# Performance work log

Hardware: AMD Instinct MI355X
Metric: run time of the kernel (lower is better)

## Reference

```python
import jax, jax.numpy as jnp
import numpy as np

# spconv.SparseConv4d(C_in, 16, (1,3,3,3), stride=1, padding=0) on spatial_shape [1000,1000,40]:
# leading kernel dim is size 1, so this is a regular (non-submanifold) 3D sparse conv,
# valid padding -> output spatial shape (998, 998, 38). Implemented as gather-GEMM-scatter:
# input point p contributes feat(p) @ W[k] to output coord p - offset[k] for each of 27 taps.

N = 200000
C_IN = 64
C_OUT = 16
K = 3
OUT_SP = (998, 998, 38)  # 1000-3+1, 1000-3+1, 40-3+1
SENT = OUT_SP[0] * OUT_SP[1] * OUT_SP[2]  # sentinel linear index for invalid taps


def setup_inputs() -> dict:
    key = jax.random.key(0)
    k1, k2, k3, k4, k5, k6 = jax.random.split(key, 6)
    feats = jax.random.normal(k1, (N, C_IN), dtype=jnp.float32)
    x = jax.random.randint(k2, (N,), 0, 1000, dtype=jnp.int32)
    y = jax.random.randint(k3, (N,), 0, 1000, dtype=jnp.int32)
    z = jax.random.randint(k4, (N,), 0, 40, dtype=jnp.int32)
    coords = jnp.stack([jnp.zeros((N,), jnp.int32), x, y, z], axis=1)  # [N,4] (b,x,y,z)
    fan_in = C_IN * K * K * K
    W = jax.random.normal(k5, (K * K * K, C_IN, C_OUT), dtype=jnp.float32) / np.sqrt(fan_in)
    bias = jax.random.normal(k6, (C_OUT,), dtype=jnp.float32) * 0.01
    return {"input": feats, "coords": coords, "W": W, "bias": bias}


def reference(input, coords, W, bias):
    # kernel tap offsets, C-order over (kx,ky,kz) in [0,3)^3 -> [27,3]
    off = jnp.stack(
        jnp.meshgrid(jnp.arange(K), jnp.arange(K), jnp.arange(K), indexing="ij"),
        axis=-1,
    ).reshape(K * K * K, 3).astype(jnp.int32)
    xyz = coords[:, 1:4]                              # [N,3]
    oc = xyz[:, None, :] - off[None, :, :]            # [N,27,3] output coord per tap
    out_sp = jnp.array(OUT_SP, dtype=jnp.int32)
    valid = jnp.all((oc >= 0) & (oc < out_sp), axis=-1)  # [N,27]
    lin = oc[..., 0] * (OUT_SP[1] * OUT_SP[2]) + oc[..., 1] * OUT_SP[2] + oc[..., 2]
    lin = jnp.where(valid, lin, SENT).reshape(-1)     # [N*27]

    # gather-GEMM: per-tap GEMM over all active voxels
    contrib = jnp.einsum("nc,kco->nko", input, W)     # [N,27,16]
    contrib = jnp.where(valid[..., None], contrib, 0.0).reshape(-1, C_OUT)

    NK = N * (K * K * K)
    uniq, inv = jnp.unique(lin, return_inverse=True, size=NK, fill_value=SENT)
    inv = inv.reshape(-1)
    # scatter-add into unique output sites
    out = jax.ops.segment_sum(contrib, inv, num_segments=NK)  # [NK,16]
    cnt = jax.ops.segment_sum(valid.reshape(-1).astype(jnp.int32), inv, num_segments=NK)
    out = out + jnp.where(cnt[:, None] > 0, bias[None, :], 0.0)
    return out, uniq
```

## Files before the change

### kernel.cpp

```cpp
#include <hip/hip_runtime.h>

#define N_PTS   200000
#define CIN     64
#define COUT    16
#define KK      27
#define SXD     998
#define SYD     998
#define SZD     38
#define STRX    (SYD*SZD)
#define SENTV   (SXD*SYD*SZD)
#define NKTOT   (N_PTS*KK)
#define NWORDS  ((SENTV+31)/32)
#define NCHUNK  ((NWORDS+255)/256)

__global__ void mark_kernel(const int* __restrict__ coords, unsigned* __restrict__ bitmap,
                            unsigned* __restrict__ multi) {
    int n = blockIdx.x * blockDim.x + threadIdx.x;
    if (n >= N_PTS) return;
    int x = coords[n*4+1], y = coords[n*4+2], z = coords[n*4+3];
    #pragma unroll
    for (int m = 0; m < KK; m++) {
        int ox = x - (m/9), oy = y - ((m/3)%3), oz = z - (m%3);
        if (ox >= 0 && ox < SXD && oy >= 0 && oy < SYD && oz >= 0 && oz < SZD) {
            int lin = ox*STRX + oy*SZD + oz;
            unsigned b = 1u << (lin & 31);
            unsigned old = atomicOr(&bitmap[lin >> 5], b);
            if (old & b) atomicOr(&multi[lin >> 5], b);
        }
    }
}

__global__ void chunk_sums_kernel(const unsigned* __restrict__ bitmap, unsigned* __restrict__ csums) {
    int w = blockIdx.x * 256 + threadIdx.x;
    unsigned c = (w < NWORDS) ? (unsigned)__popc(bitmap[w]) : 0u;
    __shared__ unsigned s[256];
    s[threadIdx.x] = c;
    __syncthreads();
    for (int off = 128; off > 0; off >>= 1) {
        if (threadIdx.x < off) s[threadIdx.x] += s[threadIdx.x + off];
        __syncthreads();
    }
    if (threadIdx.x == 0) csums[blockIdx.x] = s[0];
}

__global__ void scan_chunks_kernel(const unsigned* __restrict__ csums,
                                   unsigned* __restrict__ cprefix,
                                   unsigned* __restrict__ Uptr) {
    __shared__ unsigned s[256];
    __shared__ unsigned run_s;
    if (threadIdx.x == 0) run_s = 0;
    __syncthreads();
    for (int base = 0; base < NCHUNK; base += 256) {
        int i = base + threadIdx.x;
        unsigned v = (i < NCHUNK) ? csums[i] : 0u;
        s[threadIdx.x] = v;
        __syncthreads();
        for (int off = 1; off < 256; off <<= 1) {
            unsigned t = (threadIdx.x >= off) ? s[threadIdx.x - off] : 0u;
            __syncthreads();
            s[threadIdx.x] += t;
            __syncthreads();
        }
        unsigned run = run_s;
        if (i < NCHUNK) cprefix[i] = run + s[threadIdx.x] - v;
        unsigned tile_total = s[255];
        __syncthreads();
        if (threadIdx.x == 255) run_s = run + tile_total;
        __syncthreads();
    }
    if (threadIdx.x == 0) Uptr[0] = run_s;
}

__global__ void word_prefix_kernel(const unsigned* __restrict__ bitmap,
                                   const unsigned* __restrict__ cprefix,
                                   unsigned* __restrict__ wprefix) {
    int w = blockIdx.x * 256 + threadIdx.x;
    unsigned v = (w < NWORDS) ? (unsigned)__popc(bitmap[w]) : 0u;
    __shared__ unsigned s[256];
    s[threadIdx.x] = v;
    __syncthreads();
    for (int off = 1; off < 256; off <<= 1) {
        unsigned t = (threadIdx.x >= off) ? s[threadIdx.x - off] : 0u;
        __syncthreads();
        s[threadIdx.x] += t;
        __syncthreads();
    }
    if (w < NWORDS) wprefix[w] = cprefix[blockIdx.x] + s[threadIdx.x] - v;
}

__global__ void fill_out_kernel(float* __restrict__ out, const float* __restrict__ bias,
                                const unsigned* __restrict__ Uptr) {
    unsigned U = Uptr[0];
    unsigned i = blockIdx.x * blockDim.x + threadIdx.x;
    if (i >= (unsigned)NKTOT * 4u) return;
    unsigned row = i >> 2;
    int q = i & 3;
    float4 v;
    if (row < U) v = ((const float4*)bias)[q];
    else         v = make_float4(0.f, 0.f, 0.f, 0.f);
    ((float4*)out)[i] = v;
}

__global__ void fill_uniq_kernel(float* __restrict__ uniq) {
    unsigned i = blockIdx.x * blockDim.x + threadIdx.x;
    if (i < (unsigned)NKTOT) uniq[i] = (float)SENTV;
}

__global__ void write_uniq_kernel(const unsigned* __restrict__ bitmap,
                                  const unsigned* __restrict__ wprefix,
                                  float* __restrict__ uniq) {
    int w = blockIdx.x * 256 + threadIdx.x;
    if (w >= NWORDS) return;
    unsigned bits = bitmap[w];
    unsigned r = wprefix[w];
    while (bits) {
        int b = __ffs(bits) - 1;
        bits &= bits - 1;
        uniq[r++] = (float)(w * 32 + b);
    }
}

__launch_bounds__(256)
__global__ void scatter_mm_kernel(const float* __restrict__ feats,
                                  const int* __restrict__ coords,
                                  const float* __restrict__ W,
                                  const float* __restrict__ bias,
                                  const unsigned* __restrict__ bitmap,
                                  const unsigned* __restrict__ multi,
                                  const unsigned* __restrict__ wprefix,
                                  float* __restrict__ out) {
    int n = blockIdx.x * 256 + threadIdx.x;
    if (n >= N_PTS) return;
    int x = coords[n*4+1], y = coords[n*4+2], z = coords[n*4+3];

    float4 f[CIN/4];
    const float4* fin4 = (const float4*)(feats + (size_t)n * CIN);
    #pragma unroll
    for (int i = 0; i < CIN/4; i++) f[i] = fin4[i];

    #pragma unroll 1
    for (int m = 0; m < KK; m++) {
        int ox = x - (m/9), oy = y - ((m/3)%3), oz = z - (m%3);
        if (ox < 0 || ox >= SXD || oy < 0 || oy >= SYD || oz < 0 || oz >= SZD) continue;
        int lin = ox*STRX + oy*SZD + oz;
        unsigned word = (unsigned)lin >> 5, bit = (unsigned)lin & 31u;
        unsigned rank = wprefix[word] + (unsigned)__popc(bitmap[word] & ((1u << bit) - 1u));
        bool is_multi = (multi[word] >> bit) & 1u;

        const float* wk = W + (size_t)m * CIN * COUT;
        float acc[COUT];
        #pragma unroll
        for (int o = 0; o < COUT; o++) acc[o] = 0.f;
        #pragma unroll
        for (int c4 = 0; c4 < CIN/4; c4++) {
            float4 fv = f[c4];
            const float* wrow = wk + c4 * 4 * COUT;
            #pragma unroll
            for (int o = 0; o < COUT; o++) {
                acc[o] += fv.x * wrow[o] + fv.y * wrow[COUT + o]
                        + fv.z * wrow[2*COUT + o] + fv.w * wrow[3*COUT + o];
            }
        }

        float* dst = out + (size_t)rank * COUT;
        if (!is_multi) {
            #pragma unroll
            for (int q = 0; q < 4; q++) {
                float4 v;
                v.x = acc[q*4+0] + bias[q*4+0];
                v.y = acc[q*4+1] + bias[q*4+1];
                v.z = acc[q*4+2] + bias[q*4+2];
                v.w = acc[q*4+3] + bias[q*4+3];
                ((float4*)dst)[q] = v;
            }
        } else {
            #pragma unroll
            for (int o = 0; o < COUT; o++) atomicAdd(dst + o, acc[o]);
        }
    }
}

extern "C" void kernel_launch(void* const* d_in, const int* in_sizes, int n_in,
                              void* d_out, int out_size, void* d_ws, size_t ws_size,
                              hipStream_t stream) {
    const float* feats  = (const float*)d_in[0];
    const int*   coords = (const int*)d_in[1];
    const float* W      = (const float*)d_in[2];
    const float* bias   = (const float*)d_in[3];
    float* out  = (float*)d_out;
    float* uniq = out + (size_t)NKTOT * COUT;

    unsigned* ws      = (unsigned*)d_ws;
    unsigned* bitmap  = ws;
    unsigned* multi   = ws + NWORDS;
    unsigned* wprefix = ws + 2 * (size_t)NWORDS;
    unsigned* csums   = ws + 3 * (size_t)NWORDS;
    unsigned* cprefix = csums + NCHUNK;
    unsigned* Uptr    = cprefix + NCHUNK;

    size_t needed = ((size_t)3 * NWORDS + 2 * NCHUNK + 1) * sizeof(unsigned);
    bool have_multi = ws_size >= needed;
    if (!have_multi) {
        multi   = bitmap;
        wprefix = ws + NWORDS;
        csums   = ws + 2 * (size_t)NWORDS;
        cprefix = csums + NCHUNK;
        Uptr    = cprefix + NCHUNK;
        hipMemsetAsync(bitmap, 0, (size_t)NWORDS * sizeof(unsigned), stream);
    } else {
        hipMemsetAsync(bitmap, 0, 2 * (size_t)NWORDS * sizeof(unsigned), stream);
    }

    mark_kernel<<<(N_PTS + 255) / 256, 256, 0, stream>>>(coords, bitmap, multi);
    chunk_sums_kernel<<<NCHUNK, 256, 0, stream>>>(bitmap, csums);
    scan_chunks_kernel<<<1, 256, 0, stream>>>(csums, cprefix, Uptr);
    word_prefix_kernel<<<NCHUNK, 256, 0, stream>>>(bitmap, cprefix, wprefix);
    fill_out_kernel<<<(NKTOT * 4 + 255) / 256, 256, 0, stream>>>(out, bias, Uptr);
    fill_uniq_kernel<<<(NKTOT + 255) / 256, 256, 0, stream>>>(uniq);
    write_uniq_kernel<<<NCHUNK, 256, 0, stream>>>(bitmap, wprefix, uniq);
    scatter_mm_kernel<<<(N_PTS + 255) / 256, 256, 0, stream>>>(
        feats, coords, W, bias, bitmap, multi, wprefix, out);
}
```

Baseline: 1.410 ms.

## Batch z-taps into word masks, write only tail and multi-site bias, shrink scatter blocks

The mark kernel now sets all z-taps of an (x,y) column with one or two atomicOr calls on a contiguous bit mask, instead of one atomic per tap. The full-output bias fill is replaced by two writes: bias goes only to rows hit more than once, which are seeded inside write_uniq, and a tail kernel zero-fills rows past U with nontemporal stores. Single-hit rows are written directly by the scatter kernel. That kernel now uses 64-thread blocks, vector coordinate loads, nontemporal feature loads and stores, and bias held in registers. The aim is to cut atomic traffic and avoid rewriting the roughly 345 MB output twice, at the cost of relying on every single-hit row being written later by the scatter kernel.

Result: faster. 1.253 ms (-11.1%).

```diff
diff --git a/kernel.cpp b/kernel.cpp
--- a/kernel.cpp
+++ b/kernel.cpp
@@ -13,19 +13,39 @@
 #define NWORDS  ((SENTV+31)/32)
 #define NCHUNK  ((NWORDS+255)/256)
 
+typedef float f32x4 __attribute__((ext_vector_type(4)));
+
 __global__ void mark_kernel(const int* __restrict__ coords, unsigned* __restrict__ bitmap,
                             unsigned* __restrict__ multi) {
     int n = blockIdx.x * blockDim.x + threadIdx.x;
     if (n >= N_PTS) return;
-    int x = coords[n*4+1], y = coords[n*4+2], z = coords[n*4+3];
-    #pragma unroll
-    for (int m = 0; m < KK; m++) {
-        int ox = x - (m/9), oy = y - ((m/3)%3), oz = z - (m%3);
-        if (ox >= 0 && ox < SXD && oy >= 0 && oy < SYD && oz >= 0 && oz < SZD) {
-            int lin = ox*STRX + oy*SZD + oz;
-            unsigned b = 1u << (lin & 31);
-            unsigned old = atomicOr(&bitmap[lin >> 5], b);
-            if (old & b) atomicOr(&multi[lin >> 5], b);
+    int4 c = ((const int4*)coords)[n];
+    int x = c.y, y = c.z, z = c.w;
+    int zlo = z - 2; if (zlo < 0) zlo = 0;
+    int zhi = z;     if (zhi > SZD - 1) zhi = SZD - 1;
+    unsigned nb = (unsigned)(zhi - zlo + 1);
+    unsigned mseed = (1u << nb) - 1u;
+    #pragma unroll
+    for (int dx = 0; dx < 3; dx++) {
+        int ox = x - dx;
+        if (ox < 0 || ox >= SXD) continue;
+        #pragma unroll
+        for (int dy = 0; dy < 3; dy++) {
+            int oy = y - dy;
+            if (oy < 0 || oy >= SYD) continue;
+            int lin = ox*STRX + oy*SZD + zlo;
+            unsigned w = (unsigned)lin >> 5;
+            unsigned b = (unsigned)lin & 31u;
+            unsigned lowm = mseed << b;
+            unsigned old = atomicOr(&bitmap[w], lowm);
+            unsigned col = old & lowm;
+            if (col) atomicOr(&multi[w], col);
+            if (b + nb > 32u) {
+                unsigned highm = mseed >> (32u - b);
+                unsigned old2 = atomicOr(&bitmap[w+1], highm);
+                unsigned col2 = old2 & highm;
+                if (col2) atomicOr(&multi[w+1], col2);
+            }
         }
     }
 }
@@ -106,21 +126,48 @@
     if (i < (unsigned)NKTOT) uniq[i] = (float)SENTV;
 }
 
+__global__ void tail_kernel(float* __restrict__ out, float* __restrict__ uniq,
+                            const unsigned* __restrict__ Uptr) {
+    unsigned U = Uptr[0];
+    unsigned i = blockIdx.x * blockDim.x + threadIdx.x;
+    if (i >= (unsigned)NKTOT || i < U) return;
+    f32x4 z4 = {0.f, 0.f, 0.f, 0.f};
+    f32x4* dst = (f32x4*)(out + (size_t)i * COUT);
+    #pragma unroll
+    for (int q = 0; q < 4; q++) __builtin_nontemporal_store(z4, dst + q);
+    __builtin_nontemporal_store((float)SENTV, uniq + i);
+}
+
 __global__ void write_uniq_kernel(const unsigned* __restrict__ bitmap,
+                                  const unsigned* __restrict__ multi,
                                   const unsigned* __restrict__ wprefix,
-                                  float* __restrict__ uniq) {
+                                  float* __restrict__ uniq,
+                                  float* __restrict__ out,
+                                  const float* __restrict__ bias,
+                                  int do_bias) {
     int w = blockIdx.x * 256 + threadIdx.x;
     if (w >= NWORDS) return;
     unsigned bits = bitmap[w];
+    if (!bits) return;
+    unsigned mbits = do_bias ? multi[w] : 0u;
+    f32x4 bv[4];
+    #pragma unroll
+    for (int q = 0; q < 4; q++) bv[q] = ((const f32x4*)bias)[q];
     unsigned r = wprefix[w];
     while (bits) {
         int b = __ffs(bits) - 1;
         bits &= bits - 1;
-        uniq[r++] = (float)(w * 32 + b);
-    }
-}
-
-__launch_bounds__(256)
+        uniq[r] = (float)(w * 32 + b);
+        if ((mbits >> b) & 1u) {
+            f32x4* dst = (f32x4*)(out + (size_t)r * COUT);
+            #pragma unroll
+            for (int q = 0; q < 4; q++) __builtin_nontemporal_store(bv[q], dst + q);
+        }
+        r++;
+    }
+}
+
+__launch_bounds__(64)
 __global__ void scatter_mm_kernel(const float* __restrict__ feats,
                                   const int* __restrict__ coords,
                                   const float* __restrict__ W,
@@ -129,14 +176,19 @@
                                   const unsigned* __restrict__ multi,
                                   const unsigned* __restrict__ wprefix,
                                   float* __restrict__ out) {
-    int n = blockIdx.x * 256 + threadIdx.x;
+    int n = blockIdx.x * 64 + threadIdx.x;
     if (n >= N_PTS) return;
-    int x = coords[n*4+1], y = coords[n*4+2], z = coords[n*4+3];
-
-    float4 f[CIN/4];
-    const float4* fin4 = (const float4*)(feats + (size_t)n * CIN);
-    #pragma unroll
-    for (int i = 0; i < CIN/4; i++) f[i] = fin4[i];
+    int4 cc = ((const int4*)coords)[n];
+    int x = cc.y, y = cc.z, z = cc.w;
+
+    f32x4 f[CIN/4];
+    const f32x4* fin4 = (const f32x4*)(feats + (size_t)n * CIN);
+    #pragma unroll
+    for (int i = 0; i < CIN/4; i++) f[i] = __builtin_nontemporal_load(fin4 + i);
+
+    f32x4 bv[4];
+    #pragma unroll
+    for (int q = 0; q < 4; q++) bv[q] = ((const f32x4*)bias)[q];
 
     #pragma unroll 1
     for (int m = 0; m < KK; m++) {
@@ -153,7 +205,7 @@
         for (int o = 0; o < COUT; o++) acc[o] = 0.f;
         #pragma unroll
         for (int c4 = 0; c4 < CIN/4; c4++) {
-            float4 fv = f[c4];
+            f32x4 fv = f[c4];
             const float* wrow = wk + c4 * 4 * COUT;
             #pragma unroll
             for (int o = 0; o < COUT; o++) {
@@ -166,12 +218,12 @@
         if (!is_multi) {
             #pragma unroll
             for (int q = 0; q < 4; q++) {
-                float4 v;
-                v.x = acc[q*4+0] + bias[q*4+0];
-                v.y = acc[q*4+1] + bias[q*4+1];
-                v.z = acc[q*4+2] + bias[q*4+2];
-                v.w = acc[q*4+3] + bias[q*4+3];
-                ((float4*)dst)[q] = v;
+                f32x4 v;
+                v.x = acc[q*4+0] + bv[q].x;
+                v.y = acc[q*4+1] + bv[q].y;
+                v.z = acc[q*4+2] + bv[q].z;
+                v.w = acc[q*4+3] + bv[q].w;
+                __builtin_nontemporal_store(v, ((f32x4*)dst) + q);
             }
         } else {
             #pragma unroll
@@ -215,9 +267,16 @@
     chunk_sums_kernel<<<NCHUNK, 256, 0, stream>>>(bitmap, csums);
     scan_chunks_kernel<<<1, 256, 0, stream>>>(csums, cprefix, Uptr);
     word_prefix_kernel<<<NCHUNK, 256, 0, stream>>>(bitmap, cprefix, wprefix);
-    fill_out_kernel<<<(NKTOT * 4 + 255) / 256, 256, 0, stream>>>(out, bias, Uptr);
-    fill_uniq_kernel<<<(NKTOT + 255) / 256, 256, 0, stream>>>(uniq);
-    write_uniq_kernel<<<NCHUNK, 256, 0, stream>>>(bitmap, wprefix, uniq);
-    scatter_mm_kernel<<<(N_PTS + 255) / 256, 256, 0, stream>>>(
+
+    if (have_multi) {
+        write_uniq_kernel<<<NCHUNK, 256, 0, stream>>>(bitmap, multi, wprefix, uniq, out, bias, 1);
+        tail_kernel<<<(NKTOT + 255) / 256, 256, 0, stream>>>(out, uniq, Uptr);
+    } else {
+        fill_out_kernel<<<(NKTOT * 4 + 255) / 256, 256, 0, stream>>>(out, bias, Uptr);
+        fill_uniq_kernel<<<(NKTOT + 255) / 256, 256, 0, stream>>>(uniq);
+        write_uniq_kernel<<<NCHUNK, 256, 0, stream>>>(bitmap, multi, wprefix, uniq, out, bias, 0);
+    }
+
+    scatter_mm_kernel<<<(N_PTS + 63) / 64, 64, 0, stream>>>(
         feats, coords, W, bias, bitmap, multi, wprefix, out);
 }
```
